# Performance work log

Measured on AMD Instinct MI355X. Metric: run time of the kernel, lower is better.

The kernel has to match this reference:

```python
import jax, jax.numpy as jnp
import numpy as np

NEG_SLOPE = 0.2
EPS = 1e-16

N_NODES = 10000
N_EDGES = 80000
F_IN = 128
HID = 300
H1 = 5  # first_heads
H3 = 3  # out_head
N_CLASSES = 40


def gat_conv(x, edge_index, W, att_src, att_dst, bias, heads, out_ch, concat):
    """PyG-style GATConv (v1 attention), eval mode (no dropout).

    x: [N, F_in]; edge_index: [2, E] (row 0 = source, row 1 = target),
    self-loops already included. W: [F_in, heads*out_ch];
    att_src/att_dst: [heads, out_ch].
    """
    N = x.shape[0]
    h = (x @ W).reshape(N, heads, out_ch)            # [N, H, C]
    a_src = jnp.einsum('nhc,hc->nh', h, att_src)     # [N, H]
    a_dst = jnp.einsum('nhc,hc->nh', h, att_dst)     # [N, H]
    src, dst = edge_index[0], edge_index[1]
    e = jax.nn.leaky_relu(a_src[src] + a_dst[dst], NEG_SLOPE)  # [E, H]
    # segment softmax over incoming edges of each target node
    m = jax.ops.segment_max(e, dst, num_segments=N)  # [N, H]
    ex = jnp.exp(e - m[dst])
    s = jax.ops.segment_sum(ex, dst, num_segments=N)
    alpha = ex / (s[dst] + EPS)                      # [E, H]
    msg = h[src] * alpha[:, :, None]                 # [E, H, C]
    out = jax.ops.segment_sum(msg, dst, num_segments=N)  # [N, H, C]
    if concat:
        out = out.reshape(N, heads * out_ch)
    else:
        out = out.mean(axis=1)
    return out + bias


def setup_inputs() -> dict:
    key = jax.random.key(0)
    ks = jax.random.split(key, 12)
    glorot = lambda k, shape: jax.random.normal(k, shape, jnp.float32) * np.sqrt(
        2.0 / (shape[0] + shape[-1]))
    x = jax.random.normal(ks[0], (N_NODES, F_IN), jnp.float32)
    edge_index = jax.random.randint(ks[1], (2, N_EDGES), 0, N_NODES, jnp.int64)
    return {
        'x': x,
        'edge_index': edge_index,
        'W1': glorot(ks[2], (F_IN, H1 * HID)),
        'as1': glorot(ks[3], (H1, HID)),
        'ad1': glorot(ks[4], (H1, HID)),
        'b1': jnp.zeros((H1 * HID,), jnp.float32),
        'W2': glorot(ks[5], (H1 * HID, H1 * HID)),
        'as2': glorot(ks[6], (H1, HID)),
        'ad2': glorot(ks[7], (H1, HID)),
        'b2': jnp.zeros((H1 * HID,), jnp.float32),
        'W3': glorot(ks[8], (H1 * HID, H3 * N_CLASSES)),
        'as3': glorot(ks[9], (H3, N_CLASSES)),
        'ad3': glorot(ks[10], (H3, N_CLASSES)),
        'b3': jnp.zeros((N_CLASSES,), jnp.float32),
    }


def reference(x, edge_index, W1, as1, ad1, b1, W2, as2, ad2, b2, W3, as3, ad3, b3):
    N = x.shape[0]
    # PyG GATConv adds self-loops by default
    loops = jnp.arange(N, dtype=edge_index.dtype)
    ei = jnp.concatenate([edge_index, jnp.stack([loops, loops])], axis=1)
    # dropout layers are identity in eval mode
    h = gat_conv(x, ei, W1, as1, ad1, b1, H1, HID, True)
    h = jax.nn.elu(h)
    h2 = gat_conv(h, ei, W2, as2, ad2, b2, H1, HID, True)
    h = jax.nn.elu(h + h2)
    h = gat_conv(h, ei, W3, as3, ad3, b3, H3, N_CLASSES, False)  # [N, n_cls]
    pooled = h.sum(axis=0, keepdims=True)                        # [1, n_cls]
    return (pooled, jax.nn.log_softmax(pooled, axis=1))
```

## Files before the change

### kernel.cpp

```cpp
#include <hip/hip_runtime.h>
#include <hip/hip_bf16.h>
#include <math.h>

#define NN       10000
#define F_IN     128
#define HID      300
#define H1       5
#define H3       3
#define NCLS     40
#define HC1      (H1*HID)
#define KPAD     1536
#define HS12     304
#define NL12     1520
#define HS3      48
#define NL3      144
#define LD3      160
#define NEG_SLOPE 0.2f
#define EPSV     1e-16f

typedef __attribute__((ext_vector_type(8))) short bf16x8;
typedef __attribute__((ext_vector_type(8))) unsigned short u16x8;
typedef __attribute__((ext_vector_type(4))) float f32x4;

__device__ inline unsigned short f2bf(float f) {
  unsigned int u = __builtin_bit_cast(unsigned int, f);
  unsigned int r = (u + 0x7FFFu + ((u >> 16) & 1u)) >> 16;
  return (unsigned short)r;
}
__device__ inline float bf2f(unsigned short s) {
  unsigned int u = ((unsigned int)s) << 16;
  return __builtin_bit_cast(float, u);
}

__device__ __forceinline__ void gl2lds16(const unsigned short* g, unsigned short* l) {
  __builtin_amdgcn_global_load_lds(
      (const __attribute__((address_space(1))) unsigned int*)(const void*)g,
      (__attribute__((address_space(3))) unsigned int*)(void*)l, 16, 0, 0);
}

__global__ void k_count(const int* __restrict__ ei, int* __restrict__ counts,
                        int E0, int Etot) {
  int e = blockIdx.x * 256 + threadIdx.x;
  if (e >= Etot) return;
  int dst = (e < E0) ? ei[E0 + e] : (e - E0);
  atomicAdd(&counts[dst], 1);
}

__global__ __launch_bounds__(256) void k_scan(const int* __restrict__ counts,
                                              int* __restrict__ offsets,
                                              int* __restrict__ cursor,
                                              int N, int Etot) {
  __shared__ int sh[256];
  const int CH = 40;
  int t = threadIdx.x;
  int base = t * CH;
  int s = 0;
  for (int i = 0; i < CH; i++) {
    int idx = base + i;
    if (idx < N) s += counts[idx];
  }
  sh[t] = s;
  __syncthreads();
  for (int d = 1; d < 256; d <<= 1) {
    int v = (t >= d) ? sh[t - d] : 0;
    __syncthreads();
    sh[t] += v;
    __syncthreads();
  }
  int run = sh[t] - s;
  for (int i = 0; i < CH; i++) {
    int idx = base + i;
    if (idx < N) {
      offsets[idx] = run;
      cursor[idx] = run;
      run += counts[idx];
    }
  }
  if (t == 0) offsets[N] = Etot;
}

__global__ void k_scatter(const int* __restrict__ ei, int* __restrict__ cursor,
                          int* __restrict__ csr_src, int E0, int Etot) {
  int e = blockIdx.x * 256 + threadIdx.x;
  if (e >= Etot) return;
  int src, dst;
  if (e < E0) { src = ei[e]; dst = ei[E0 + e]; }
  else        { src = dst = e - E0; }
  int pos = atomicAdd(&cursor[dst], 1);
  csr_src[pos] = src;
}

__global__ void k_cvt(const float* __restrict__ in, unsigned short* __restrict__ out,
                      int R, int C, int Cpad) {
  long long idx = (long long)blockIdx.x * 256 + threadIdx.x;
  if (idx >= (long long)R * Cpad) return;
  int r = (int)(idx / Cpad), c = (int)(idx - (long long)r * Cpad);
  out[idx] = (c < C) ? f2bf(in[(size_t)r * C + c]) : 0;
}

__global__ void k_attpad3(const float* __restrict__ as1, const float* __restrict__ ad1,
                          const float* __restrict__ as2, const float* __restrict__ ad2,
                          const float* __restrict__ as3, const float* __restrict__ ad3,
                          float* __restrict__ ps1, float* __restrict__ pd1,
                          float* __restrict__ ps2, float* __restrict__ pd2,
                          float* __restrict__ ps3, float* __restrict__ pd3) {
  int i = blockIdx.x * 256 + threadIdx.x;
  if (i < KPAD) {
    int h = i / HS12, cin = i - h * HS12;
    bool live = (h < H1) && (cin < HID);
    int o = live ? (h * HID + cin) : 0;
    ps1[i] = live ? as1[o] : 0.f;
    pd1[i] = live ? ad1[o] : 0.f;
    ps2[i] = live ? as2[o] : 0.f;
    pd2[i] = live ? ad2[o] : 0.f;
  }
  if (i < LD3) {
    int h = i / HS3, cin = i - h * HS3;
    bool live = (h < H3) && (cin < NCLS);
    ps3[i] = live ? as3[h * NCLS + cin] : 0.f;
    pd3[i] = live ? ad3[h * NCLS + cin] : 0.f;
  }
}

__global__ __launch_bounds__(256) void k_cvtT(const float* __restrict__ in,
                                              unsigned short* __restrict__ out,
                                              int K, int Nm, int kC, int kS, int Kp,
                                              int nC, int nS, int Nmp) {
  __shared__ float tile[64][65];
  int k0 = blockIdx.y * 64, n0 = blockIdx.x * 64;
  int c = threadIdx.x & 63, r = threadIdx.x >> 6;
  for (int rr = r; rr < 64; rr += 4) {
    int kp = k0 + rr;
    int np = n0 + c;
    float v = 0.f;
    if (kp < Kp && np < Nmp) {
      int ck = kp % kS, bk = kp / kS;
      int cn = np % nS, bn_ = np / nS;
      int ko = bk * kC + ck, no = bn_ * nC + cn;
      if (ck < kC && ko < K && cn < nC && no < Nm) v = in[(size_t)ko * Nm + no];
    }
    tile[rr][c] = v;
  }
  __syncthreads();
  for (int rr = r; rr < 64; rr += 4) {
    int np = n0 + rr, kp = k0 + c;
    if (np < Nmp && kp < Kp) out[(size_t)np * Kp + kp] = f2bf(tile[c][rr]);
  }
}

#define BM 256
#define BN 128
#define BK 64

__global__ __launch_bounds__(512) void gemm_mfma(
    const unsigned short* __restrict__ A,
    const unsigned short* __restrict__ Bt,
    unsigned short* __restrict__ Cbf,
    int M, int Kpad, int Nmat, int ldc, int klen, int nT,
    float* __restrict__ Cacc) {
  __shared__ unsigned short As[BM * BK];
  __shared__ unsigned short Bs[BN * BK];
  int tid = threadIdx.x;
  int lane = tid & 63, wid = tid >> 6;
  int wm = wid >> 1, wn = wid & 1;
  int bid = blockIdx.x;
  int slot = bid & 7, idx = bid >> 3;
  int nTi = idx % nT, mg = idx / nT;
  int bm = (slot + 8 * mg) * BM, bn = nTi * BN;
  int quad = lane >> 4, l16 = lane & 15;
  int kq = quad * 8;
  int koff = blockIdx.y * klen;

  int ar0 = min(bm + 32 * wid + l16, M - 1);
  int ar1 = min(bm + 32 * wid + 16 + l16, M - 1);
  int br0 = min(bn + 16 * wid + l16, Nmat - 1);
  const unsigned short* gA0 = A + (size_t)ar0 * Kpad + kq;
  const unsigned short* gA1 = A + (size_t)ar1 * Kpad + kq;
  const unsigned short* gB0 = Bt + (size_t)br0 * Kpad + kq;
  unsigned short* lA = As + 4 * wid * 512;
  unsigned short* lB = Bs + 2 * wid * 512;

  f32x4 acc[4][4] = {};

  for (int kt = koff; kt < koff + klen; kt += BK) {
    gl2lds16(gA0 + kt,      lA);
    gl2lds16(gA0 + kt + 32, lA + 512);
    gl2lds16(gA1 + kt,      lA + 1024);
    gl2lds16(gA1 + kt + 32, lA + 1536);
    gl2lds16(gB0 + kt,      lB);
    gl2lds16(gB0 + kt + 32, lB + 512);
    __syncthreads();
#pragma unroll
    for (int kh = 0; kh < 2; kh++) {
      bf16x8 af[4], bfr[4];
#pragma unroll
      for (int i = 0; i < 4; i++) {
        af[i]  = *(const bf16x8*)(As + ((wm * 4 + i) * 2 + kh) * 512 + lane * 8);
        bfr[i] = *(const bf16x8*)(Bs + ((wn * 4 + i) * 2 + kh) * 512 + lane * 8);
      }
#pragma unroll
      for (int i = 0; i < 4; i++)
#pragma unroll
        for (int j = 0; j < 4; j++)
          acc[i][j] = __builtin_amdgcn_mfma_f32_16x16x32_bf16(af[i], bfr[j], acc[i][j], 0, 0, 0);
    }
    __syncthreads();
  }

#pragma unroll
  for (int i = 0; i < 4; i++) {
    int rowb = bm + wm * 64 + i * 16 + quad * 4;
#pragma unroll
    for (int j = 0; j < 4; j++) {
      int col = bn + wn * 64 + j * 16 + l16;
      if (col < ldc) {
        bool live = col < Nmat;
        if (Cacc) {
#pragma unroll
          for (int r = 0; r < 4; r++) {
            int row = rowb + r;
            if (live && row < M) atomicAdd(&Cacc[(size_t)row * ldc + col], acc[i][j][r]);
          }
        } else {
#pragma unroll
          for (int r = 0; r < 4; r++) {
            int row = rowb + r;
            if (row < M) Cbf[(size_t)row * ldc + col] = live ? f2bf(acc[i][j][r]) : 0;
          }
        }
      }
    }
  }
}

__global__ void k_att(unsigned short* __restrict__ hfeat, int ldh,
                      const float* __restrict__ attp_s,
                      const float* __restrict__ attp_d,
                      float* __restrict__ asrc, float* __restrict__ adst,
                      int H, int HS, const float* __restrict__ Cacc, int Nlive) {
  int n = blockIdx.x, t = threadIdx.x;
  __shared__ float s_ps[8], s_pd[8];
  if (t < 8) { s_ps[t] = 0.f; s_pd[t] = 0.f; }
  __syncthreads();
  int col0 = t * 8;
  if (col0 < ldh) {
    int hj = col0 / HS;
    float ps = 0.f, pd = 0.f;
    if (Cacc) {
      const float4* p = (const float4*)(Cacc + (size_t)n * ldh + col0);
      float4 f0 = p[0], f1 = p[1];
      float fv[8] = {f0.x, f0.y, f0.z, f0.w, f1.x, f1.y, f1.z, f1.w};
      u16x8 st;
#pragma unroll
      for (int j = 0; j < 8; j++) {
        bool live = (col0 + j) < Nlive;
        float v = live ? fv[j] : 0.f;
        st[j] = live ? f2bf(v) : 0;
        ps += v * attp_s[col0 + j];
        pd += v * attp_d[col0 + j];
      }
      *(u16x8*)(hfeat + (size_t)n * ldh + col0) = st;
    } else {
      u16x8 rv = *(const u16x8*)(hfeat + (size_t)n * ldh + col0);
#pragma unroll
      for (int j = 0; j < 8; j++) {
        float v = bf2f(rv[j]);
        ps += v * attp_s[col0 + j];
        pd += v * attp_d[col0 + j];
      }
    }
    atomicAdd(&s_ps[hj], ps);
    atomicAdd(&s_pd[hj], pd);
  }
  __syncthreads();
  if (t < H) {
    asrc[(size_t)n * H + t] = s_ps[t];
    adst[(size_t)n * H + t] = s_pd[t];
  }
}

__global__ void k_stats(const float* __restrict__ asrc,
                        const float* __restrict__ adst,
                        const int* __restrict__ csr_src,
                        const int* __restrict__ offsets,
                        float* __restrict__ alpha, int N, int H) {
  int t = blockIdx.x * 256 + threadIdx.x;
  if (t >= N * H) return;
  int n = t / H, h = t - n * H;
  int s0 = offsets[n], s1 = offsets[n + 1];
  float ad = adst[t];
  float m = -1e30f;
  for (int p = s0; p < s1; p++) {
    float v = asrc[csr_src[p] * H + h] + ad;
    v = v > 0.f ? v : NEG_SLOPE * v;
    m = fmaxf(m, v);
  }
  float sum = 0.f;
  for (int p = s0; p < s1; p++) {
    float v = asrc[csr_src[p] * H + h] + ad;
    v = v > 0.f ? v : NEG_SLOPE * v;
    float ex = expf(v - m);
    alpha[(size_t)p * 8 + h] = ex;
    sum += ex;
  }
  float r = 1.f / (sum + EPSV);
  for (int p = s0; p < s1; p++) alpha[(size_t)p * 8 + h] *= r;
}

__global__ __launch_bounds__(64) void k_agg(
    const unsigned short* __restrict__ hfeat, int ldh,
    const float* __restrict__ alpha,
    const int* __restrict__ csr_src,
    const int* __restrict__ offsets,
    const float* __restrict__ bias,
    const unsigned short* __restrict__ prevbf,
    unsigned short* __restrict__ out_bf,
    const float* __restrict__ b3,
    float* __restrict__ h3,
    int HS, int C, int H, int mode) {
  int n = blockIdx.x;
  int t = threadIdx.x;
  int s0 = offsets[n], s1 = offsets[n + 1];
  int col0 = blockIdx.y * 512 + t * 8;
  bool active = col0 < ldh;
  int hj = active ? (col0 / HS) : 0;
  int cbase = col0 - hj * HS;
  float acc[8] = {};

  __shared__ int s_src[64];
  __shared__ float s_alpha[64 * 8];
  __shared__ float s_out[LD3];

  for (int base = s0; base < s1; base += 64) {
    int chunk = min(64, s1 - base);
    if (t < chunk) s_src[t] = csr_src[base + t];
    for (int i = t; i < chunk * 8; i += 64) {
      int e = i >> 3, h = i & 7;
      s_alpha[i] = (h < H) ? alpha[(size_t)(base + e) * 8 + h] : 0.f;
    }
    __syncthreads();
    if (active) {
      u16x8 rv = *(const u16x8*)(hfeat + (size_t)s_src[0] * ldh + col0);
      for (int e = 0; e < chunk; e++) {
        u16x8 cur = rv;
        if (e + 1 < chunk)
          rv = *(const u16x8*)(hfeat + (size_t)s_src[e + 1] * ldh + col0);
        float al = s_alpha[e * 8 + hj];
#pragma unroll
        for (int j = 0; j < 8; j++) acc[j] += al * bf2f(cur[j]);
      }
    }
    __syncthreads();
  }

  if (mode == 2) {
    if (active) {
#pragma unroll
      for (int j = 0; j < 8; j++) s_out[col0 + j] = acc[j];
    }
    __syncthreads();
    if (t < NCLS)
      h3[(size_t)n * NCLS + t] =
          (s_out[t] + s_out[HS + t] + s_out[2 * HS + t]) * (1.f / 3.f) + b3[t];
    return;
  }

  if (!active) return;
#pragma unroll
  for (int j = 0; j < 8; j++) {
    int cin = cbase + j;
    bool live = (hj < H) && (cin < C);
    float v = 0.f;
    if (live) {
      v = acc[j] + bias[hj * C + cin];
      if (mode == 1) v += bf2f(prevbf[(size_t)n * ldh + col0 + j]);
      v = v > 0.f ? v : (expf(v) - 1.f);
    }
    out_bf[(size_t)n * ldh + col0 + j] = live ? f2bf(v) : 0;
  }
}

__global__ void k_pool(const float* __restrict__ h3, float* __restrict__ pooled,
                       int N) {
  int col = threadIdx.x;
  if (col >= NCLS) return;
  int row = blockIdx.x * 4 + threadIdx.y;
  int stride = gridDim.x * 4;
  float acc = 0.f;
  for (int r = row; r < N; r += stride) acc += h3[(size_t)r * NCLS + col];
  atomicAdd(&pooled[col], acc);
}

__global__ __launch_bounds__(64) void k_final(const float* __restrict__ pooled,
                                              float* __restrict__ out) {
  int t = threadIdx.x;
  float v = (t < NCLS) ? pooled[t] : -INFINITY;
  float m = v;
  for (int o = 32; o > 0; o >>= 1) m = fmaxf(m, __shfl_xor(m, o));
  float ex = (t < NCLS) ? expf(v - m) : 0.f;
  float s = ex;
  for (int o = 32; o > 0; o >>= 1) s += __shfl_xor(s, o);
  float lse = m + logf(s);
  if (t < NCLS) {
    out[t] = v;
    out[NCLS + t] = v - lse;
  }
}

extern "C" void kernel_launch(void* const* d_in, const int* in_sizes, int n_in,
                              void* d_out, int out_size, void* d_ws, size_t ws_size,
                              hipStream_t stream) {
  const float* x   = (const float*)d_in[0];
  const int*   ei  = (const int*)d_in[1];
  const float* W1  = (const float*)d_in[2];
  const float* as1 = (const float*)d_in[3];
  const float* ad1 = (const float*)d_in[4];
  const float* b1  = (const float*)d_in[5];
  const float* W2  = (const float*)d_in[6];
  const float* as2 = (const float*)d_in[7];
  const float* ad2 = (const float*)d_in[8];
  const float* b2  = (const float*)d_in[9];
  const float* W3  = (const float*)d_in[10];
  const float* as3 = (const float*)d_in[11];
  const float* ad3 = (const float*)d_in[12];
  const float* b3  = (const float*)d_in[13];
  float* out = (float*)d_out;

  const int N = NN;
  const int E0 = in_sizes[1] / 2;
  const int Etot = E0 + N;
  const int mT = (N + BM - 1) / BM;

  float* f = (float*)d_ws;
  float* asrc   = f;
  float* adst   = asrc + (size_t)N * H1;
  float* alphab = adst + (size_t)N * H1;
  float* pooled = alphab + (size_t)Etot * 8;
  float* h3     = pooled + 64;
  float* attps1 = h3 + (size_t)N * NCLS;
  float* attpd1 = attps1 + KPAD;
  float* attps2 = attpd1 + KPAD;
  float* attpd2 = attps2 + KPAD;
  float* attps3 = attpd2 + KPAD;
  float* attpd3 = attps3 + LD3;
  float* Cacc   = attpd3 + LD3;
  int* counts  = (int*)(Cacc + (size_t)N * LD3);
  int* offsets = counts + N;
  int* cursor  = offsets + N + 1;
  int* csr_src = cursor + N;
  uintptr_t pp = (uintptr_t)(csr_src + Etot);
  pp = (pp + 15) & ~(uintptr_t)15;
  unsigned short* hfbf = (unsigned short*)pp;
  unsigned short* abf  = hfbf + (size_t)N * KPAD;
  unsigned short* btbf = abf + (size_t)N * KPAD;

  hipMemsetAsync(counts, 0, (size_t)N * sizeof(int), stream);
  hipMemsetAsync(pooled, 0, 64 * sizeof(float), stream);

  k_count<<<(Etot + 255) / 256, 256, 0, stream>>>(ei, counts, E0, Etot);
  k_scan<<<1, 256, 0, stream>>>(counts, offsets, cursor, N, Etot);
  k_scatter<<<(Etot + 255) / 256, 256, 0, stream>>>(ei, cursor, csr_src, E0, Etot);
  k_attpad3<<<(KPAD + 255) / 256, 256, 0, stream>>>(as1, ad1, as2, ad2, as3, ad3,
                                                    attps1, attpd1, attps2, attpd2,
                                                    attps3, attpd3);

  {
    k_cvt<<<((long long)N * F_IN + 255) / 256, 256, 0, stream>>>(x, abf, N, F_IN, F_IN);
    dim3 tg((NL12 + 63) / 64, (F_IN + 63) / 64);
    k_cvtT<<<tg, 256, 0, stream>>>(W1, btbf, F_IN, HC1, F_IN, F_IN, F_IN, HID, HS12, NL12);
    int nT = (NL12 + BN - 1) / BN;
    gemm_mfma<<<dim3(nT * mT, 1), 512, 0, stream>>>(abf, btbf, hfbf, N, F_IN, NL12,
                                                    KPAD, F_IN, nT, nullptr);
    k_att<<<N, 192, 0, stream>>>(hfbf, KPAD, attps1, attpd1, asrc, adst, H1, HS12,
                                 nullptr, 0);
    k_stats<<<(N * H1 + 255) / 256, 256, 0, stream>>>(asrc, adst, csr_src, offsets,
                                                      alphab, N, H1);
    k_agg<<<dim3(N, 3), 64, 0, stream>>>(hfbf, KPAD, alphab, csr_src, offsets, b1,
                                         nullptr, abf, nullptr, nullptr,
                                         HS12, HID, H1, 0);
  }

  {
    dim3 tg((NL12 + 63) / 64, KPAD / 64);
    k_cvtT<<<tg, 256, 0, stream>>>(W2, btbf, HC1, HC1, HID, HS12, KPAD, HID, HS12, NL12);
    int nT = (NL12 + BN - 1) / BN;
    gemm_mfma<<<dim3(nT * mT, 1), 512, 0, stream>>>(abf, btbf, hfbf, N, KPAD, NL12,
                                                    KPAD, KPAD, nT, nullptr);
    k_att<<<N, 192, 0, stream>>>(hfbf, KPAD, attps2, attpd2, asrc, adst, H1, HS12,
                                 nullptr, 0);
    k_stats<<<(N * H1 + 255) / 256, 256, 0, stream>>>(asrc, adst, csr_src, offsets,
                                                      alphab, N, H1);
    k_agg<<<dim3(N, 3), 64, 0, stream>>>(hfbf, KPAD, alphab, csr_src, offsets, b2,
                                         abf, abf, nullptr, nullptr,
                                         HS12, HID, H1, 1);
  }

  {
    dim3 tg((NL3 + 63) / 64, KPAD / 64);
    k_cvtT<<<tg, 256, 0, stream>>>(W3, btbf, HC1, H3 * NCLS, HID, HS12, KPAD, NCLS, HS3, NL3);
    hipMemsetAsync(Cacc, 0, (size_t)N * LD3 * sizeof(float), stream);
    int nT = (LD3 + BN - 1) / BN;
    gemm_mfma<<<dim3(nT * mT, 4), 512, 0, stream>>>(abf, btbf, nullptr, N, KPAD, NL3,
                                                    LD3, KPAD / 4, nT, Cacc);
    k_att<<<N, 64, 0, stream>>>(hfbf, LD3, attps3, attpd3, asrc, adst, H3, HS3,
                                Cacc, NL3);
    k_stats<<<(N * H3 + 255) / 256, 256, 0, stream>>>(asrc, adst, csr_src, offsets,
                                                      alphab, N, H3);
    k_agg<<<dim3(N, 1), 64, 0, stream>>>(hfbf, LD3, alphab, csr_src, offsets, nullptr,
                                         nullptr, nullptr, b3, h3,
                                         HS3, NCLS, H3, 2);
  }

  k_pool<<<64, dim3(64, 4), 0, stream>>>(h3, pooled, N);
  k_final<<<1, 64, 0, stream>>>(pooled, out);
}
```

Measured before the change: 573.0 us.

## Fuse softmax stats into aggregation kernel and shrink GEMM tile to 128x128

Removes the separate k_stats kernel and the alpha buffer. Each aggregation block now computes an online max and sum over its incoming edges per head and recomputes alpha on the fly. Separately, the GEMM block tile drops from 256x128 with 512 threads to 128x128 with 256 threads, and mT is hardcoded to 80 so more blocks launch. The cost is that softmax stats are recomputed redundantly across the y-blocks of k_agg (3 for layers 1 and 2), plus extra expf work in exchange for avoiding the alpha round trip through global memory.

Measured after the change: 552.5 us. 3.6% less time.

```diff
diff --git a/kernel.cpp b/kernel.cpp
--- a/kernel.cpp
+++ b/kernel.cpp
@@ -148,11 +148,11 @@
   }
 }
 
-#define BM 256
+#define BM 128
 #define BN 128
 #define BK 64
 
-__global__ __launch_bounds__(512) void gemm_mfma(
+__global__ __launch_bounds__(256) void gemm_mfma(
     const unsigned short* __restrict__ A,
     const unsigned short* __restrict__ Bt,
     unsigned short* __restrict__ Cbf,
@@ -171,14 +171,16 @@
   int kq = quad * 8;
   int koff = blockIdx.y * klen;
 
-  int ar0 = min(bm + 32 * wid + l16, M - 1);
-  int ar1 = min(bm + 32 * wid + 16 + l16, M - 1);
-  int br0 = min(bn + 16 * wid + l16, Nmat - 1);
+  int ar0 = min(bm + (2 * wid) * 16 + l16, M - 1);
+  int ar1 = min(bm + (2 * wid + 1) * 16 + l16, M - 1);
+  int br0 = min(bn + (2 * wid) * 16 + l16, Nmat - 1);
+  int br1 = min(bn + (2 * wid + 1) * 16 + l16, Nmat - 1);
   const unsigned short* gA0 = A + (size_t)ar0 * Kpad + kq;
   const unsigned short* gA1 = A + (size_t)ar1 * Kpad + kq;
   const unsigned short* gB0 = Bt + (size_t)br0 * Kpad + kq;
+  const unsigned short* gB1 = Bt + (size_t)br1 * Kpad + kq;
   unsigned short* lA = As + 4 * wid * 512;
-  unsigned short* lB = Bs + 2 * wid * 512;
+  unsigned short* lB = Bs + 4 * wid * 512;
 
   f32x4 acc[4][4] = {};
 
@@ -189,6 +191,8 @@
     gl2lds16(gA1 + kt + 32, lA + 1536);
     gl2lds16(gB0 + kt,      lB);
     gl2lds16(gB0 + kt + 32, lB + 512);
+    gl2lds16(gB1 + kt,      lB + 1024);
+    gl2lds16(gB1 + kt + 32, lB + 1536);
     __syncthreads();
 #pragma unroll
     for (int kh = 0; kh < 2; kh++) {
@@ -279,37 +283,10 @@
   }
 }
 
-__global__ void k_stats(const float* __restrict__ asrc,
-                        const float* __restrict__ adst,
-                        const int* __restrict__ csr_src,
-                        const int* __restrict__ offsets,
-                        float* __restrict__ alpha, int N, int H) {
-  int t = blockIdx.x * 256 + threadIdx.x;
-  if (t >= N * H) return;
-  int n = t / H, h = t - n * H;
-  int s0 = offsets[n], s1 = offsets[n + 1];
-  float ad = adst[t];
-  float m = -1e30f;
-  for (int p = s0; p < s1; p++) {
-    float v = asrc[csr_src[p] * H + h] + ad;
-    v = v > 0.f ? v : NEG_SLOPE * v;
-    m = fmaxf(m, v);
-  }
-  float sum = 0.f;
-  for (int p = s0; p < s1; p++) {
-    float v = asrc[csr_src[p] * H + h] + ad;
-    v = v > 0.f ? v : NEG_SLOPE * v;
-    float ex = expf(v - m);
-    alpha[(size_t)p * 8 + h] = ex;
-    sum += ex;
-  }
-  float r = 1.f / (sum + EPSV);
-  for (int p = s0; p < s1; p++) alpha[(size_t)p * 8 + h] *= r;
-}
-
 __global__ __launch_bounds__(64) void k_agg(
     const unsigned short* __restrict__ hfeat, int ldh,
-    const float* __restrict__ alpha,
+    const float* __restrict__ asrc,
+    const float* __restrict__ adst,
     const int* __restrict__ csr_src,
     const int* __restrict__ offsets,
     const float* __restrict__ bias,
@@ -321,22 +298,58 @@
   int n = blockIdx.x;
   int t = threadIdx.x;
   int s0 = offsets[n], s1 = offsets[n + 1];
+
+  __shared__ float s_ad[8], s_pm[64], s_pl[64], s_mx[8], s_rinv[8];
+  __shared__ int s_src[64];
+  __shared__ float s_alpha[64 * 8];
+  __shared__ float s_out[LD3];
+
+  if (t < 8) s_ad[t] = (t < H) ? adst[(size_t)n * H + t] : 0.f;
+  __syncthreads();
+
+  int hh = t & 7, sl = t >> 3;
+  float m = -1e30f, l = 0.f;
+  if (hh < H) {
+    float ad = s_ad[hh];
+    for (int p = s0 + sl; p < s1; p += 8) {
+      float v = asrc[csr_src[p] * H + hh] + ad;
+      v = v > 0.f ? v : NEG_SLOPE * v;
+      if (v > m) { l = l * expf(m - v) + 1.f; m = v; }
+      else       { l += expf(v - m); }
+    }
+  }
+  s_pm[t] = m; s_pl[t] = l;
+  __syncthreads();
+  if (t < 8) {
+    float M2 = -1e30f, L2 = 0.f;
+    for (int k = 0; k < 8; k++) {
+      float mk = s_pm[t + 8 * k], lk = s_pl[t + 8 * k];
+      if (mk > M2) { L2 = L2 * expf(M2 - mk) + lk; M2 = mk; }
+      else         { L2 += lk * expf(mk - M2); }
+    }
+    s_mx[t] = M2;
+    s_rinv[t] = 1.f / (L2 + EPSV);
+  }
+  __syncthreads();
+
   int col0 = blockIdx.y * 512 + t * 8;
   bool active = col0 < ldh;
   int hj = active ? (col0 / HS) : 0;
   int cbase = col0 - hj * HS;
   float acc[8] = {};
 
-  __shared__ int s_src[64];
-  __shared__ float s_alpha[64 * 8];
-  __shared__ float s_out[LD3];
-
   for (int base = s0; base < s1; base += 64) {
     int chunk = min(64, s1 - base);
     if (t < chunk) s_src[t] = csr_src[base + t];
     for (int i = t; i < chunk * 8; i += 64) {
       int e = i >> 3, h = i & 7;
-      s_alpha[i] = (h < H) ? alpha[(size_t)(base + e) * 8 + h] : 0.f;
+      float a = 0.f;
+      if (h < H) {
+        float v = asrc[csr_src[base + e] * H + h] + s_ad[h];
+        v = v > 0.f ? v : NEG_SLOPE * v;
+        a = expf(v - s_mx[h]) * s_rinv[h];
+      }
+      s_alpha[i] = a;
     }
     __syncthreads();
     if (active) {
@@ -429,13 +442,12 @@
   const int N = NN;
   const int E0 = in_sizes[1] / 2;
   const int Etot = E0 + N;
-  const int mT = (N + BM - 1) / BM;
+  const int mT = 80;
 
   float* f = (float*)d_ws;
   float* asrc   = f;
   float* adst   = asrc + (size_t)N * H1;
-  float* alphab = adst + (size_t)N * H1;
-  float* pooled = alphab + (size_t)Etot * 8;
+  float* pooled = adst + (size_t)N * H1;
   float* h3     = pooled + 64;
   float* attps1 = h3 + (size_t)N * NCLS;
   float* attpd1 = attps1 + KPAD;
@@ -469,14 +481,12 @@
     dim3 tg((NL12 + 63) / 64, (F_IN + 63) / 64);
     k_cvtT<<<tg, 256, 0, stream>>>(W1, btbf, F_IN, HC1, F_IN, F_IN, F_IN, HID, HS12, NL12);
     int nT = (NL12 + BN - 1) / BN;
-    gemm_mfma<<<dim3(nT * mT, 1), 512, 0, stream>>>(abf, btbf, hfbf, N, F_IN, NL12,
+    gemm_mfma<<<dim3(nT * mT, 1), 256, 0, stream>>>(abf, btbf, hfbf, N, F_IN, NL12,
                                                     KPAD, F_IN, nT, nullptr);
     k_att<<<N, 192, 0, stream>>>(hfbf, KPAD, attps1, attpd1, asrc, adst, H1, HS12,
                                  nullptr, 0);
-    k_stats<<<(N * H1 + 255) / 256, 256, 0, stream>>>(asrc, adst, csr_src, offsets,
-                                                      alphab, N, H1);
-    k_agg<<<dim3(N, 3), 64, 0, stream>>>(hfbf, KPAD, alphab, csr_src, offsets, b1,
-                                         nullptr, abf, nullptr, nullptr,
+    k_agg<<<dim3(N, 3), 64, 0, stream>>>(hfbf, KPAD, asrc, adst, csr_src, offsets,
+                                         b1, nullptr, abf, nullptr, nullptr,
                                          HS12, HID, H1, 0);
   }
 
@@ -484,14 +494,12 @@
     dim3 tg((NL12 + 63) / 64, KPAD / 64);
     k_cvtT<<<tg, 256, 0, stream>>>(W2, btbf, HC1, HC1, HID, HS12, KPAD, HID, HS12, NL12);
     int nT = (NL12 + BN - 1) / BN;
-    gemm_mfma<<<dim3(nT * mT, 1), 512, 0, stream>>>(abf, btbf, hfbf, N, KPAD, NL12,
+    gemm_mfma<<<dim3(nT * mT, 1), 256, 0, stream>>>(abf, btbf, hfbf, N, KPAD, NL12,
                                                     KPAD, KPAD, nT, nullptr);
     k_att<<<N, 192, 0, stream>>>(hfbf, KPAD, attps2, attpd2, asrc, adst, H1, HS12,
                                  nullptr, 0);
-    k_stats<<<(N * H1 + 255) / 256, 256, 0, stream>>>(asrc, adst, csr_src, offsets,
-                                                      alphab, N, H1);
-    k_agg<<<dim3(N, 3), 64, 0, stream>>>(hfbf, KPAD, alphab, csr_src, offsets, b2,
-                                         abf, abf, nullptr, nullptr,
+    k_agg<<<dim3(N, 3), 64, 0, stream>>>(hfbf, KPAD, asrc, adst, csr_src, offsets,
+                                         b2, abf, abf, nullptr, nullptr,
                                          HS12, HID, H1, 1);
   }
 
@@ -500,14 +508,12 @@
     k_cvtT<<<tg, 256, 0, stream>>>(W3, btbf, HC1, H3 * NCLS, HID, HS12, KPAD, NCLS, HS3, NL3);
     hipMemsetAsync(Cacc, 0, (size_t)N * LD3 * sizeof(float), stream);
     int nT = (LD3 + BN - 1) / BN;
-    gemm_mfma<<<dim3(nT * mT, 4), 512, 0, stream>>>(abf, btbf, nullptr, N, KPAD, NL3,
+    gemm_mfma<<<dim3(nT * mT, 4), 256, 0, stream>>>(abf, btbf, nullptr, N, KPAD, NL3,
                                                     LD3, KPAD / 4, nT, Cacc);
     k_att<<<N, 64, 0, stream>>>(hfbf, LD3, attps3, attpd3, asrc, adst, H3, HS3,
                                 Cacc, NL3);
-    k_stats<<<(N * H3 + 255) / 256, 256, 0, stream>>>(asrc, adst, csr_src, offsets,
-                                                      alphab, N, H3);
-    k_agg<<<dim3(N, 1), 64, 0, stream>>>(hfbf, LD3, alphab, csr_src, offsets, nullptr,
-                                         nullptr, nullptr, b3, h3,
+    k_agg<<<dim3(N, 1), 64, 0, stream>>>(hfbf, LD3, asrc, adst, csr_src, offsets,
+                                         nullptr, nullptr, nullptr, b3, h3,
                                          HS3, NCLS, H3, 2);
   }
 
```
